# Kernel optimization log

Measured on AMD Instinct MI355X. Metric: run time of the kernel, lower is better.

## Reference

```python
import jax, jax.numpy as jnp
import numpy as np

B, IN, HID, OUT, MH = 32, 784, 256, 128, 32
RATE = 1e-3


def setup_inputs() -> dict:
    key = jax.random.key(0)
    ks = jax.random.split(key, 6)
    def w(k, shape, fan_in):
        return (jax.random.normal(k, shape, jnp.float32) / np.sqrt(fan_in)).astype(jnp.float32)
    return {
        "x": jax.random.normal(ks[0], (B, IN), jnp.float32),
        "W1": w(ks[1], (HID, IN), IN),
        "b1": jnp.zeros((HID,), jnp.float32),
        "W2": w(ks[2], (OUT, HID), HID),
        "b2": jnp.zeros((OUT,), jnp.float32),
        "mW1": w(ks[3], (MH, 3), 3),
        "mb1": jnp.zeros((MH,), jnp.float32),
        "mW2": w(ks[4], (1, MH), MH),
        "mb2": jnp.zeros((1,), jnp.float32),
        "batch_num": 1,
    }


def _meta(feats, mW1, mb1, mW2, mb2):
    # feats: [B, O, I, 3] -> scalar shift per (b, j, i)
    h = jax.nn.relu(jnp.einsum("boif,hf->boih", feats, mW1) + mb1)
    return (jnp.einsum("boih,kh->boik", h, mW2) + mb2)[..., 0]  # [B, O, I]


def _layer_step(out, W, b, mW1, mb1, mW2, mb2, scale):
    vi = out                                   # [B, I]
    vj = jax.nn.relu(out @ W.T + b)            # [B, O]
    # features per (batch, out-neuron, in-neuron): (input act, weight, output act)
    feats = jnp.stack(
        jnp.broadcast_arrays(vi[:, None, :], W[None, :, :], vj[:, :, None]),
        axis=-1,
    )  # [B, O, I, 3]
    shift = _meta(feats, mW1, mb1, mW2, mb2) * scale   # [B, O, I]
    new_out = vj + jnp.einsum("bi,boi->bo", vi, shift)  # weighted reduce over inputs
    W_new = W + jnp.mean(shift, axis=0)                 # hebbian-style weight update
    return new_out, W_new


def reference(x, W1, b1, W2, b2, mW1, mb1, mW2, mb2, batch_num):
    scale = RATE / batch_num
    out1, W1_new = _layer_step(x, W1, b1, mW1, mb1, mW2, mb2, scale)
    out2, W2_new = _layer_step(out1, W2, b2, mW1, mb1, mW2, mb2, scale)
    return out2, W1_new, W2_new
```

## Files before the change

### kernel.cpp

```cpp
#include <hip/hip_runtime.h>

#define B_   32
#define IN_  784
#define HID_ 256
#define OUT_ 128
#define MH_  32
#define RATE_ 1e-3f

#define OFF_OUT1  0
#define OFF_XT    8192
#define OFF_O1T   33280
#define OFF_VJ1T  41472
#define OFF_VJ2T  49664

__global__ void kA(const float* __restrict__ x, const float* __restrict__ W1,
                   const float* __restrict__ b1, float* __restrict__ ws) {
    float* out1 = ws + OFF_OUT1;
    float* xT   = ws + OFF_XT;
    float* vjT1 = ws + OFF_VJ1T;
    int t = threadIdx.x, blk = blockIdx.x;

    if (blk < 98) {
        int e = blk * 256 + t;
        int i = e >> 5, b = e & 31;
        xT[e] = x[b * IN_ + i];
    }

    int lane = t & 63;
    int p = blk * 4 + (t >> 6);
    int b = p >> 8, o = p & 255;
    const float4* xr4 = (const float4*)(x  + b * IN_);
    const float4* wr4 = (const float4*)(W1 + o * IN_);
    float acc = 0.f;
    #pragma unroll
    for (int k = 0; k < 3; ++k) {
        float4 xa = xr4[lane + 64 * k];
        float4 wa = wr4[lane + 64 * k];
        acc = fmaf(xa.x, wa.x, acc); acc = fmaf(xa.y, wa.y, acc);
        acc = fmaf(xa.z, wa.z, acc); acc = fmaf(xa.w, wa.w, acc);
    }
    if (lane < 4) {
        float4 xa = xr4[192 + lane];
        float4 wa = wr4[192 + lane];
        acc = fmaf(xa.x, wa.x, acc); acc = fmaf(xa.y, wa.y, acc);
        acc = fmaf(xa.z, wa.z, acc); acc = fmaf(xa.w, wa.w, acc);
    }
    #pragma unroll
    for (int m = 1; m < 64; m <<= 1) acc += __shfl_xor(acc, m, 64);
    if (lane == 0) {
        float v = fmaxf(acc + b1[o], 0.f);
        out1[p] = v;
        vjT1[o * 32 + b] = v;
    }
}

template<int IN_DIM, int OUT_DIM, int NCH, int CPT>
__global__ __launch_bounds__(256)
void layer_main(const float* __restrict__ viT,
                const float* __restrict__ W,
                const float* __restrict__ vjT,
                const float* __restrict__ mW1, const float* __restrict__ mb1,
                const float* __restrict__ mW2, const float* __restrict__ mb2,
                const int*   __restrict__ batch_num,
                float* __restrict__ Wnew,
                float* __restrict__ outAcc)
{
    __shared__ float4 m4s[MH_];
    __shared__ float  w2s[MH_];
    __shared__ float  osh[4][32];

    int t = threadIdx.x;
    int b = t & 31, g = t >> 5;
    int o  = blockIdx.x / NCH;
    int i0 = (blockIdx.x % NCH) * (8 * CPT) + g * CPT;

    if (t < MH_) {
        m4s[t] = make_float4(mW1[t*3+0], mW1[t*3+1], mW1[t*3+2], mb1[t]);
        w2s[t] = mW2[t];
    }
    __syncthreads();

    float vjv = vjT[o * 32 + b];

    float vi[CPT], wv[CPT], s[CPT];
    #pragma unroll
    for (int k = 0; k < CPT; ++k) {
        vi[k] = viT[(i0 + k) * 32 + b];
        wv[k] = W[o * IN_DIM + i0 + k];
        s[k]  = 0.f;
    }

    #pragma unroll
    for (int hc = 0; hc < MH_ / 8; ++hc) {
        float a[8], bw[8], w2[8], cvm[8];
        #pragma unroll
        for (int j = 0; j < 8; ++j) {
            float4 m = m4s[hc * 8 + j];
            a[j]   = m.x;
            bw[j]  = m.y;
            cvm[j] = fmaf(m.z, vjv, m.w);
            w2[j]  = w2s[hc * 8 + j];
        }
        #pragma unroll
        for (int k = 0; k < CPT; ++k) {
            float vik = vi[k], wvk = wv[k];
            #pragma unroll
            for (int j = 0; j < 8; ++j) {
                float tt = fmaf(a[j], vik, fmaf(bw[j], wvk, cvm[j]));
                tt = fmaxf(tt, 0.f);
                s[k] = fmaf(w2[j], tt, s[k]);
            }
        }
    }

    float scale = RATE_ / (float)batch_num[0];
    float mb2v  = mb2[0];
    float outacc = 0.f;
    float r[CPT];
    #pragma unroll
    for (int k = 0; k < CPT; ++k) {
        float sh = (s[k] + mb2v) * scale;
        outacc = fmaf(vi[k], sh, outacc);
        r[k] = sh;
    }
    #pragma unroll
    for (int mm = 1; mm < 32; mm <<= 1) {
        #pragma unroll
        for (int k = 0; k < CPT; ++k) r[k] += __shfl_xor(r[k], mm);
    }
    if (b == 0) {
        #pragma unroll
        for (int k = 0; k < CPT; ++k)
            Wnew[o * IN_DIM + i0 + k] = wv[k] + r[k] * 0.03125f;
    }

    outacc += __shfl_xor(outacc, 32);
    if ((t & 32) == 0) osh[t >> 6][b] = outacc;
    __syncthreads();
    if (t < 32) {
        float v = osh[0][t] + osh[1][t] + osh[2][t] + osh[3][t];
        atomicAdd(&outAcc[t * OUT_DIM + o], v);
    }
}

__global__ void kC(const float* __restrict__ out1, const float* __restrict__ W2,
                   const float* __restrict__ b2, float* __restrict__ vj2T,
                   float* __restrict__ o1T, float* __restrict__ out2) {
    int t = threadIdx.x, blk = blockIdx.x;

    if (blk < 32) {
        int e = blk * 256 + t;
        int i = e >> 5, b = e & 31;
        o1T[e] = out1[b * HID_ + i];
    }

    int lane = t & 63;
    int p = blk * 4 + (t >> 6);
    int b = p >> 7, o = p & 127;
    const float4* xr4 = (const float4*)(out1 + b * HID_);
    const float4* wr4 = (const float4*)(W2   + o * HID_);
    float4 xa = xr4[lane];
    float4 wa = wr4[lane];
    float acc = fmaf(xa.x, wa.x, fmaf(xa.y, wa.y, fmaf(xa.z, wa.z, xa.w * wa.w)));
    #pragma unroll
    for (int m = 1; m < 64; m <<= 1) acc += __shfl_xor(acc, m, 64);
    if (lane == 0) {
        float v = fmaxf(acc + b2[o], 0.f);
        out2[p]          = v;
        vj2T[o * 32 + b] = v;
    }
}

extern "C" void kernel_launch(void* const* d_in, const int* in_sizes, int n_in,
                              void* d_out, int out_size, void* d_ws, size_t ws_size,
                              hipStream_t stream) {
    const float* x   = (const float*)d_in[0];
    const float* W1  = (const float*)d_in[1];
    const float* b1  = (const float*)d_in[2];
    const float* W2  = (const float*)d_in[3];
    const float* b2  = (const float*)d_in[4];
    const float* mW1 = (const float*)d_in[5];
    const float* mb1 = (const float*)d_in[6];
    const float* mW2 = (const float*)d_in[7];
    const float* mb2 = (const float*)d_in[8];
    const int* batch_num = (const int*)d_in[9];

    float* out2  = (float*)d_out;
    float* W1n   = out2 + B_ * OUT_;
    float* W2n   = W1n + HID_ * IN_;
    float* ws    = (float*)d_ws;

    kA<<<2048, 256, 0, stream>>>(x, W1, b1, ws);
    layer_main<IN_, HID_, 7, 14><<<HID_ * 7, 256, 0, stream>>>(
        ws + OFF_XT, W1, ws + OFF_VJ1T, mW1, mb1, mW2, mb2, batch_num,
        W1n, ws + OFF_OUT1);
    kC<<<1024, 256, 0, stream>>>(ws + OFF_OUT1, W2, b2,
                                 ws + OFF_VJ2T, ws + OFF_O1T, out2);
    layer_main<HID_, OUT_, 8, 4><<<OUT_ * 8, 256, 0, stream>>>(
        ws + OFF_O1T, W2, ws + OFF_VJ2T, mW1, mb1, mW2, mb2, batch_num,
        W2n, out2);
}
```

Baseline: 110.8 us.

## Fuse layer-2 matvec into meta kernel and drop transposed activation copies

```diff
diff --git a/kernel.cpp b/kernel.cpp
--- a/kernel.cpp
+++ b/kernel.cpp
@@ -8,45 +8,37 @@
 #define RATE_ 1e-3f
 
 #define OFF_OUT1  0
-#define OFF_XT    8192
-#define OFF_O1T   33280
-#define OFF_VJ1T  41472
-#define OFF_VJ2T  49664
-
-__global__ void kA(const float* __restrict__ x, const float* __restrict__ W1,
-                   const float* __restrict__ b1, float* __restrict__ ws) {
-    float* out1 = ws + OFF_OUT1;
-    float* xT   = ws + OFF_XT;
-    float* vjT1 = ws + OFF_VJ1T;
-    int t = threadIdx.x, blk = blockIdx.x;
-
-    if (blk < 98) {
-        int e = blk * 256 + t;
-        int i = e >> 5, b = e & 31;
-        xT[e] = x[b * IN_ + i];
-    }
-
-    int lane = t & 63;
-    int p = blk * 4 + (t >> 6);
-    int b = p >> 8, o = p & 255;
-    const float4* xr4 = (const float4*)(x  + b * IN_);
-    const float4* wr4 = (const float4*)(W1 + o * IN_);
+#define OFF_VJ1T  8192
+
+template<int NQ, int TAIL>
+__device__ __forceinline__ float waveDot(const float4* __restrict__ a,
+                                         const float4* __restrict__ c, int lane) {
     float acc = 0.f;
     #pragma unroll
-    for (int k = 0; k < 3; ++k) {
-        float4 xa = xr4[lane + 64 * k];
-        float4 wa = wr4[lane + 64 * k];
+    for (int k = 0; k < NQ; ++k) {
+        float4 xa = a[lane + 64 * k], wa = c[lane + 64 * k];
         acc = fmaf(xa.x, wa.x, acc); acc = fmaf(xa.y, wa.y, acc);
         acc = fmaf(xa.z, wa.z, acc); acc = fmaf(xa.w, wa.w, acc);
     }
-    if (lane < 4) {
-        float4 xa = xr4[192 + lane];
-        float4 wa = wr4[192 + lane];
+    if (TAIL > 0 && lane < TAIL) {
+        float4 xa = a[NQ * 64 + lane], wa = c[NQ * 64 + lane];
         acc = fmaf(xa.x, wa.x, acc); acc = fmaf(xa.y, wa.y, acc);
         acc = fmaf(xa.z, wa.z, acc); acc = fmaf(xa.w, wa.w, acc);
     }
     #pragma unroll
     for (int m = 1; m < 64; m <<= 1) acc += __shfl_xor(acc, m, 64);
+    return acc;
+}
+
+__global__ void kA2(const float* __restrict__ x, const float* __restrict__ W1,
+                    const float* __restrict__ b1, float* __restrict__ ws) {
+    float* out1 = ws + OFF_OUT1;
+    float* vjT1 = ws + OFF_VJ1T;
+    int t = threadIdx.x, lane = t & 63;
+    int p = blockIdx.x * 4 + (t >> 6);
+    int b = p >> 8, o = p & 255;
+    float acc = waveDot<3, 4>((const float4*)(x + b * IN_),
+                              (const float4*)(W1 + o * IN_), lane);
     if (lane == 0) {
         float v = fmaxf(acc + b1[o], 0.f);
         out1[p] = v;
@@ -56,7 +48,7 @@
 
 template<int IN_DIM, int OUT_DIM, int NCH, int CPT>
 __global__ __launch_bounds__(256)
-void layer_main(const float* __restrict__ viT,
+void layer_meta(const float* __restrict__ viRow,
                 const float* __restrict__ W,
                 const float* __restrict__ vjT,
                 const float* __restrict__ mW1, const float* __restrict__ mb1,
@@ -83,11 +75,18 @@
     float vjv = vjT[o * 32 + b];
 
     float vi[CPT], wv[CPT], s[CPT];
-    #pragma unroll
-    for (int k = 0; k < CPT; ++k) {
-        vi[k] = viT[(i0 + k) * 32 + b];
-        wv[k] = W[o * IN_DIM + i0 + k];
-        s[k]  = 0.f;
+    {
+        const float* xr = viRow + b * IN_DIM + i0;
+        const float* wr = W     + o * IN_DIM + i0;
+        #pragma unroll
+        for (int k = 0; k < CPT / 2; ++k) {
+            float2 v2 = *(const float2*)(xr + 2 * k);
+            float2 w2v = *(const float2*)(wr + 2 * k);
+            vi[2*k] = v2.x; vi[2*k+1] = v2.y;
+            wv[2*k] = w2v.x; wv[2*k+1] = w2v.y;
+        }
+        #pragma unroll
+        for (int k = 0; k < CPT; ++k) s[k] = 0.f;
     }
 
     #pragma unroll
@@ -143,31 +142,110 @@
     }
 }
 
-__global__ void kC(const float* __restrict__ out1, const float* __restrict__ W2,
-                   const float* __restrict__ b2, float* __restrict__ vj2T,
-                   float* __restrict__ o1T, float* __restrict__ out2) {
-    int t = threadIdx.x, blk = blockIdx.x;
-
-    if (blk < 32) {
-        int e = blk * 256 + t;
-        int i = e >> 5, b = e & 31;
-        o1T[e] = out1[b * HID_ + i];
-    }
-
-    int lane = t & 63;
-    int p = blk * 4 + (t >> 6);
-    int b = p >> 7, o = p & 127;
-    const float4* xr4 = (const float4*)(out1 + b * HID_);
-    const float4* wr4 = (const float4*)(W2   + o * HID_);
-    float4 xa = xr4[lane];
-    float4 wa = wr4[lane];
-    float acc = fmaf(xa.x, wa.x, fmaf(xa.y, wa.y, fmaf(xa.z, wa.z, xa.w * wa.w)));
-    #pragma unroll
-    for (int m = 1; m < 64; m <<= 1) acc += __shfl_xor(acc, m, 64);
-    if (lane == 0) {
-        float v = fmaxf(acc + b2[o], 0.f);
-        out2[p]          = v;
-        vj2T[o * 32 + b] = v;
+__global__ __launch_bounds__(256)
+void layer2_fused(const float* __restrict__ out1,
+                  const float* __restrict__ W2,
+                  const float* __restrict__ b2,
+                  const float* __restrict__ mW1, const float* __restrict__ mb1,
+                  const float* __restrict__ mW2, const float* __restrict__ mb2,
+                  const int*   __restrict__ batch_num,
+                  float* __restrict__ W2n,
+                  float* __restrict__ out2)
+{
+    __shared__ float4 m4s[MH_];
+    __shared__ float  w2s[MH_];
+    __shared__ float  osh[4][32];
+    __shared__ float  vjsh[32];
+
+    int t = threadIdx.x;
+    int lane = t & 63, wid = t >> 6;
+    int o = blockIdx.x >> 2, chunk = blockIdx.x & 3;
+
+    if (t < MH_) {
+        m4s[t] = make_float4(mW1[t*3+0], mW1[t*3+1], mW1[t*3+2], mb1[t]);
+        w2s[t] = mW2[t];
+    }
+
+    #pragma unroll
+    for (int q = 0; q < 8; ++q) {
+        int bv = wid * 8 + q;
+        float acc = waveDot<1, 0>((const float4*)(out1 + bv * HID_),
+                                  (const float4*)(W2 + o * HID_), lane);
+        if (lane == 0) vjsh[bv] = fmaxf(acc + b2[o], 0.f);
+    }
+    __syncthreads();
+
+    int b = t & 31, g = t >> 5;
+    constexpr int CPT = 8;
+    int i0 = chunk * 64 + g * CPT;
+
+    float vjv = vjsh[b];
+    float vi[CPT], wv[CPT], s[CPT];
+    {
+        const float* xr = out1 + b * HID_ + i0;
+        const float* wr = W2   + o * HID_ + i0;
+        #pragma unroll
+        for (int k = 0; k < CPT / 2; ++k) {
+            float2 v2 = *(const float2*)(xr + 2 * k);
+            float2 w2v = *(const float2*)(wr + 2 * k);
+            vi[2*k] = v2.x; vi[2*k+1] = v2.y;
+            wv[2*k] = w2v.x; wv[2*k+1] = w2v.y;
+        }
+        #pragma unroll
+        for (int k = 0; k < CPT; ++k) s[k] = 0.f;
+    }
+
+    #pragma unroll
+    for (int hc = 0; hc < MH_ / 8; ++hc) {
+        float a[8], bw[8], w2[8], cvm[8];
+        #pragma unroll
+        for (int j = 0; j < 8; ++j) {
+            float4 m = m4s[hc * 8 + j];
+            a[j]   = m.x;
+            bw[j]  = m.y;
+            cvm[j] = fmaf(m.z, vjv, m.w);
+            w2[j]  = w2s[hc * 8 + j];
+        }
+        #pragma unroll
+        for (int k = 0; k < CPT; ++k) {
+            float vik = vi[k], wvk = wv[k];
+            #pragma unroll
+            for (int j = 0; j < 8; ++j) {
+                float tt = fmaf(a[j], vik, fmaf(bw[j], wvk, cvm[j]));
+                tt = fmaxf(tt, 0.f);
+                s[k] = fmaf(w2[j], tt, s[k]);
+            }
+        }
+    }
+
+    float scale = RATE_ / (float)batch_num[0];
+    float mb2v  = mb2[0];
+    float outacc = 0.f;
+    float r[CPT];
+    #pragma unroll
+    for (int k = 0; k < CPT; ++k) {
+        float sh = (s[k] + mb2v) * scale;
+        outacc = fmaf(vi[k], sh, outacc);
+        r[k] = sh;
+    }
+    #pragma unroll
+    for (int mm = 1; mm < 32; mm <<= 1) {
+        #pragma unroll
+        for (int k = 0; k < CPT; ++k) r[k] += __shfl_xor(r[k], mm);
+    }
+    if (b == 0) {
+        #pragma unroll
+        for (int k = 0; k < CPT; ++k)
+            W2n[o * HID_ + i0 + k] = wv[k] + r[k] * 0.03125f;
+    }
+
+    outacc += __shfl_xor(outacc, 32);
+    if ((t & 32) == 0) osh[t >> 6][b] = outacc;
+    __syncthreads();
+    if (t < 32) {
+        float v = osh[0][t] + osh[1][t] + osh[2][t] + osh[3][t];
+        if (chunk == 0) v += vjsh[t];
+        atomicAdd(&out2[t * OUT_ + o], v);
     }
 }
 
@@ -185,18 +263,17 @@
     const float* mb2 = (const float*)d_in[8];
     const int* batch_num = (const int*)d_in[9];
 
-    float* out2  = (float*)d_out;
-    float* W1n   = out2 + B_ * OUT_;
-    float* W2n   = W1n + HID_ * IN_;
-    float* ws    = (float*)d_ws;
-
-    kA<<<2048, 256, 0, stream>>>(x, W1, b1, ws);
-    layer_main<IN_, HID_, 7, 14><<<HID_ * 7, 256, 0, stream>>>(
-        ws + OFF_XT, W1, ws + OFF_VJ1T, mW1, mb1, mW2, mb2, batch_num,
+    float* out2 = (float*)d_out;
+    float* W1n  = out2 + B_ * OUT_;
+    float* W2n  = W1n + HID_ * IN_;
+    float* ws   = (float*)d_ws;
+
+    hipMemsetAsync(out2, 0, B_ * OUT_ * sizeof(float), stream);
+    kA2<<<2048, 256, 0, stream>>>(x, W1, b1, ws);
+    layer_meta<IN_, HID_, 7, 14><<<HID_ * 7, 256, 0, stream>>>(
+        x, W1, ws + OFF_VJ1T, mW1, mb1, mW2, mb2, batch_num,
         W1n, ws + OFF_OUT1);
-    kC<<<1024, 256, 0, stream>>>(ws + OFF_OUT1, W2, b2,
-                                 ws + OFF_VJ2T, ws + OFF_O1T, out2);
-    layer_main<HID_, OUT_, 8, 4><<<OUT_ * 8, 256, 0, stream>>>(
-        ws + OFF_O1T, W2, ws + OFF_VJ2T, mW1, mb1, mW2, mb2, batch_num,
+    layer2_fused<<<OUT_ * 4, 256, 0, stream>>>(
+        ws + OFF_OUT1, W2, b2, mW1, mb1, mW2, mb2, batch_num,
         W2n, out2);
 }
```

Measured after the change: 111.2 us. No clear change (+0.4%).
